# Kernel tuning notes

Measured on AMD Instinct MI355X. Metric: run time of the kernel, lower is better.

## Reference

```python
import jax, jax.numpy as jnp
import numpy as np


def setup_inputs() -> dict:
    key = jax.random.key(0)
    k1, k2, k3, k4 = jax.random.split(key, 4)
    B, T, E, H = 8, 2048, 1024, 64
    x = jax.random.normal(k1, (B, T, E), dtype=jnp.float32)
    # scale params like typical init to keep logits sane
    Wk = jax.random.normal(k2, (E, H), dtype=jnp.float32) * (E ** -0.5)
    Wq = jax.random.normal(k3, (E, H), dtype=jnp.float32) * (E ** -0.5)
    Wv = jax.random.normal(k4, (E, H), dtype=jnp.float32) * (E ** -0.5)
    return {"x": x, "Wk": Wk, "Wq": Wq, "Wv": Wv}


def reference(x, Wk, Wq, Wv):
    # x: [B, T, E]; Wk/Wq/Wv: [E, H]
    T = x.shape[1]
    H = Wk.shape[1]
    k = jnp.einsum('bte,eh->bth', x, Wk)
    q = jnp.einsum('bte,eh->bth', x, Wq)
    v = jnp.einsum('bte,eh->bth', x, Wv)
    # scaled scores [B, T, T]
    wei = jnp.einsum('bqh,bkh->bqk', q, k) * (H ** -0.5)
    causal = jnp.tril(jnp.ones((T, T), dtype=bool))  # tril buffer
    wei = jnp.where(causal, wei, -jnp.inf)
    wei = jax.nn.softmax(wei, axis=-1)
    # dropout p=0.0 (eval): identity
    return jnp.einsum('bqk,bkh->bqh', wei, v)
```

## Files before the change

kernel.cpp:

```cpp
#include <hip/hip_runtime.h>
#include <math.h>

constexpr int B_ = 8, T_ = 2048, E_ = 1024, H_ = 64;
constexpr long BT = (long)B_ * T_;

typedef __attribute__((ext_vector_type(8))) short bf16x8;
typedef __attribute__((ext_vector_type(4))) float f32x4;

__device__ inline unsigned short bf16_rne(float f) {
    union { float f; unsigned u; } v; v.f = f;
    unsigned u = v.u + (0x7FFFu + ((v.u >> 16) & 1u));
    return (unsigned short)(u >> 16);
}
__device__ inline unsigned pack_bf16x2(float lo, float hi) {
    return (unsigned)bf16_rne(lo) | ((unsigned)bf16_rne(hi) << 16);
}

constexpr float QS = 0.18033688011112042f;

__global__ __launch_bounds__(256) void wt_build_k(
    const float* __restrict__ Wk, const float* __restrict__ Wq,
    const float* __restrict__ Wv, unsigned short* __restrict__ Wt)
{
    const int d    = blockIdx.x * 256 + threadIdx.x;
    const int tile = d >> 6;
    const int lq   = d & 63;
    const int quad = lq >> 4;
    const int l16  = lq & 15;
    const int kc   = tile / 12;
    const int nt   = tile - kc * 12;
    const int n    = nt * 16 + l16;

    const float* src; int col; float s = 1.0f;
    if (n < 64)       { src = Wk; col = n; }
    else if (n < 128) { src = Wq; col = n - 64; s = QS; }
    else              { src = Wv; col = n - 128; }

    const int kk0 = kc * 32 + quad * 8;
    const float* sp = src + (size_t)kk0 * H_ + col;
    unsigned p[4];
    #pragma unroll
    for (int jj = 0; jj < 4; jj++)
        p[jj] = pack_bf16x2(sp[(2 * jj) * H_] * s, sp[(2 * jj + 1) * H_] * s);
    *(uint4*)(Wt + (size_t)d * 8) = make_uint4(p[0], p[1], p[2], p[3]);
}

__global__ __launch_bounds__(512, 4) void qkv_mfma_k(
    const float* __restrict__ x, const unsigned short* __restrict__ Wt,
    unsigned short* __restrict__ kO, unsigned short* __restrict__ qO,
    unsigned short* __restrict__ vfO)
{
    __shared__ unsigned short VL[32][66];

    const int t    = threadIdx.x;
    const int w    = t >> 6;
    const int l    = t & 63;
    const int l16  = l & 15;
    const int quad = l >> 4;
    const int rg   = w >> 2;
    const int nq   = w & 3;
    const int row0 = blockIdx.x * 32 + rg * 16;

    const float* xp = x + (size_t)(row0 + l16) * E_ + quad * 8;
    const unsigned short* wp = Wt + (size_t)(nq * 3) * 512 + (size_t)l * 8;

    f32x4 acc[3];
    #pragma unroll
    for (int n = 0; n < 3; n++) acc[n] = (f32x4){0.f, 0.f, 0.f, 0.f};

    float4 a0 = *(const float4*)(xp);
    float4 a1 = *(const float4*)(xp + 4);
    bf16x8 bf[3];
    #pragma unroll
    for (int n = 0; n < 3; n++) bf[n] = *(const bf16x8*)(wp + (size_t)n * 512);

    for (int kc = 0; kc < 32; ++kc) {
        const int kn = (kc + 1) & 31;
        float4 na0 = *(const float4*)(xp + kn * 32);
        float4 na1 = *(const float4*)(xp + kn * 32 + 4);
        bf16x8 nb[3];
        #pragma unroll
        for (int n = 0; n < 3; n++)
            nb[n] = *(const bf16x8*)(wp + (size_t)(kn * 12 + n) * 512);

        union { bf16x8 v; unsigned u[4]; } av;
        av.u[0] = pack_bf16x2(a0.x, a0.y);
        av.u[1] = pack_bf16x2(a0.z, a0.w);
        av.u[2] = pack_bf16x2(a1.x, a1.y);
        av.u[3] = pack_bf16x2(a1.z, a1.w);

        #pragma unroll
        for (int n = 0; n < 3; n++)
            acc[n] = __builtin_amdgcn_mfma_f32_16x16x32_bf16(av.v, bf[n], acc[n], 0, 0, 0);

        a0 = na0; a1 = na1;
        #pragma unroll
        for (int n = 0; n < 3; n++) bf[n] = nb[n];
    }

    #pragma unroll
    for (int n = 0; n < 3; n++) {
        const int gn = nq * 3 + n;
        const int hb = gn * 16 + l16;
        if (gn < 4) {
            #pragma unroll
            for (int r = 0; r < 4; r++) {
                const int row = row0 + quad * 4 + r;
                kO[(size_t)row * H_ + hb] = bf16_rne(acc[n][r]);
            }
        } else if (gn < 8) {
            #pragma unroll
            for (int r = 0; r < 4; r++) {
                const int row = row0 + quad * 4 + r;
                qO[(size_t)row * H_ + (hb - 64)] = bf16_rne(acc[n][r]);
            }
        } else {
            #pragma unroll
            for (int r = 0; r < 4; r++)
                VL[rg * 16 + quad * 4 + r][(gn - 8) * 16 + l16] = bf16_rne(acc[n][r]);
        }
    }
    __syncthreads();

    if (t < 256) {
        const int g  = t >> 6;
        const int lf = t & 15;
        const int qf = (t >> 4) & 3;
        unsigned pk[4];
        #pragma unroll
        for (int jj = 0; jj < 4; jj++) {
            const int p0 = qf * 8 + 2 * jj;
            const int i0 = (p0 >> 1) | ((p0 & 1) << 4);
            const int p1 = p0 + 1;
            const int i1 = (p1 >> 1) | ((p1 & 1) << 4);
            pk[jj] = (unsigned)VL[i0][g * 16 + lf]
                   | ((unsigned)VL[i1][g * 16 + lf] << 16);
        }
        const int tile = blockIdx.x;
        *(uint4*)(vfO + ((size_t)tile * 4 + g) * 512 + (size_t)(t & 63) * 8) =
            make_uint4(pk[0], pk[1], pk[2], pk[3]);
    }
}

__global__ __launch_bounds__(256, 4) void attn_mfma(
    const unsigned short* __restrict__ q,
    const unsigned short* __restrict__ k,
    const unsigned short* __restrict__ vf,
    float* __restrict__ out)
{
    __shared__ unsigned short Pl[4][16 * 40];
    __shared__ float Ot[4][16][68];
    __shared__ float lsW[4][16];

    const int t    = threadIdx.x;
    const int w    = t >> 6;
    const int l    = t & 63;
    const int l16  = l & 15;
    const int quad = l >> 4;

    const int b    = blockIdx.x & 7;
    const int qidx = blockIdx.x >> 3;
    const int qt   = (qidx & 1) ? (127 - (qidx >> 1)) : (qidx >> 1);
    const int t0   = qt * 16;
    const int nk   = t0 / 32 + 1;

    const size_t qoff = ((size_t)b * T_ + t0 + l16) * H_ + quad * 8;
    bf16x8 aq0 = *(const bf16x8*)(q + qoff);
    bf16x8 aq1 = *(const bf16x8*)(q + qoff + 32);

    f32x4 o[4];
    #pragma unroll
    for (int g = 0; g < 4; g++) o[g] = (f32x4){0.f, 0.f, 0.f, 0.f};
    float ls[4] = {0.f, 0.f, 0.f, 0.f};

    const unsigned short* kbp = k + (size_t)b * T_ * H_;
    const unsigned short* vbp = vf + (size_t)b * 64 * 2048 + (size_t)l * 8;
    unsigned short* Pw = &Pl[w][0];

    bf16x8 bk00, bk01, bk10, bk11, bv0, bv1, bv2, bv3;
    if (w < nk) {
        const int kbase = w * 32;
        const unsigned short* kp = kbp + (size_t)(kbase + l16) * H_ + quad * 8;
        bk00 = *(const bf16x8*)(kp);
        bk01 = *(const bf16x8*)(kp + 32);
        bk10 = *(const bf16x8*)(kp + 16 * H_);
        bk11 = *(const bf16x8*)(kp + 16 * H_ + 32);
        const unsigned short* vp = vbp + (size_t)w * 2048;
        bv0 = *(const bf16x8*)(vp);
        bv1 = *(const bf16x8*)(vp + 512);
        bv2 = *(const bf16x8*)(vp + 1024);
        bv3 = *(const bf16x8*)(vp + 1536);
    }

    for (int kt = w; kt < nk; kt += 4) {
        const int ktn    = (kt + 4 < nk) ? kt + 4 : kt;
        const int kbasen = ktn * 32;
        const unsigned short* kpn = kbp + (size_t)(kbasen + l16) * H_ + quad * 8;
        bf16x8 nk00 = *(const bf16x8*)(kpn);
        bf16x8 nk01 = *(const bf16x8*)(kpn + 32);
        bf16x8 nk10 = *(const bf16x8*)(kpn + 16 * H_);
        bf16x8 nk11 = *(const bf16x8*)(kpn + 16 * H_ + 32);
        const unsigned short* vpn = vbp + (size_t)ktn * 2048;
        bf16x8 nv0 = *(const bf16x8*)(vpn);
        bf16x8 nv1 = *(const bf16x8*)(vpn + 512);
        bf16x8 nv2 = *(const bf16x8*)(vpn + 1024);
        bf16x8 nv3 = *(const bf16x8*)(vpn + 1536);

        const int kbase = kt * 32;
        f32x4 s0 = (f32x4){0.f, 0.f, 0.f, 0.f};
        f32x4 s1 = (f32x4){0.f, 0.f, 0.f, 0.f};
        s0 = __builtin_amdgcn_mfma_f32_16x16x32_bf16(aq0, bk00, s0, 0, 0, 0);
        s0 = __builtin_amdgcn_mfma_f32_16x16x32_bf16(aq1, bk01, s0, 0, 0, 0);
        s1 = __builtin_amdgcn_mfma_f32_16x16x32_bf16(aq0, bk10, s1, 0, 0, 0);
        s1 = __builtin_amdgcn_mfma_f32_16x16x32_bf16(aq1, bk11, s1, 0, 0, 0);

        if (kbase + 31 > t0) {
            const int rowb = t0 + quad * 4;
            #pragma unroll
            for (int r = 0; r < 4; r++) {
                if (kbase + l16 > rowb + r)      s0[r] = -3.0e38f;
                if (kbase + 16 + l16 > rowb + r) s1[r] = -3.0e38f;
            }
        }

        #pragma unroll
        for (int r = 0; r < 4; r++) {
            float p0 = exp2f(s0[r]);
            float p1 = exp2f(s1[r]);
            ls[r] += p0 + p1;
            *(unsigned*)(Pw + (quad * 4 + r) * 40 + 2 * l16) = pack_bf16x2(p0, p1);
        }
        asm volatile("s_waitcnt lgkmcnt(0)" ::: "memory");
        bf16x8 ap = *(const bf16x8*)(Pw + l16 * 40 + quad * 8);

        o[0] = __builtin_amdgcn_mfma_f32_16x16x32_bf16(ap, bv0, o[0], 0, 0, 0);
        o[1] = __builtin_amdgcn_mfma_f32_16x16x32_bf16(ap, bv1, o[1], 0, 0, 0);
        o[2] = __builtin_amdgcn_mfma_f32_16x16x32_bf16(ap, bv2, o[2], 0, 0, 0);
        o[3] = __builtin_amdgcn_mfma_f32_16x16x32_bf16(ap, bv3, o[3], 0, 0, 0);

        bk00 = nk00; bk01 = nk01; bk10 = nk10; bk11 = nk11;
        bv0 = nv0; bv1 = nv1; bv2 = nv2; bv3 = nv3;
    }

    #pragma unroll
    for (int r = 0; r < 4; r++) {
        float s = ls[r];
        s += __shfl_xor(s, 1);
        s += __shfl_xor(s, 2);
        s += __shfl_xor(s, 4);
        s += __shfl_xor(s, 8);
        ls[r] = s;
    }
    if (l16 == 0) {
        #pragma unroll
        for (int r = 0; r < 4; r++) lsW[w][quad * 4 + r] = ls[r];
    }
    #pragma unroll
    for (int g = 0; g < 4; g++)
        #pragma unroll
        for (int r = 0; r < 4; r++)
            Ot[w][quad * 4 + r][g * 16 + l16] = o[g][r];
    __syncthreads();

    {
        const int col = w * 16 + l16;
        #pragma unroll
        for (int r = 0; r < 4; r++) {
            const int row = quad * 4 + r;
            float L  = lsW[0][row] + lsW[1][row] + lsW[2][row] + lsW[3][row];
            float sv = Ot[0][row][col] + Ot[1][row][col]
                     + Ot[2][row][col] + Ot[3][row][col];
            out[((size_t)b * T_ + t0 + row) * H_ + col] = sv / L;
        }
    }
}

extern "C" void kernel_launch(void* const* d_in, const int* in_sizes, int n_in,
                              void* d_out, int out_size, void* d_ws, size_t ws_size,
                              hipStream_t stream)
{
    const float* x  = (const float*)d_in[0];
    const float* Wk = (const float*)d_in[1];
    const float* Wq = (const float*)d_in[2];
    const float* Wv = (const float*)d_in[3];

    unsigned short* wt    = (unsigned short*)d_ws;
    unsigned short* kbuf  = wt + 24576 * 8;
    unsigned short* qbuf  = kbuf + BT * H_;
    unsigned short* vfbuf = qbuf + BT * H_;
    float* outp = (float*)d_out;

    wt_build_k<<<96, 256, 0, stream>>>(Wk, Wq, Wv, wt);
    qkv_mfma_k<<<(B_ * T_) / 32, 512, 0, stream>>>(x, wt, kbuf, qbuf, vfbuf);
    attn_mfma<<<B_ * 128, 256, 0, stream>>>(qbuf, kbuf, vfbuf, outp);
}
```

Before: 168.7 us.

## Stage x tiles in LDS via async global_load_lds with double buffering

The QKV projection kernel now copies each 32x64 fp32 tile of x into shared memory with global_load_lds, using a double buffer and an XOR swizzle, instead of having each wave load its own x fragments from global memory straight into registers. Previously the four waves covering different output column groups each fetched the same x rows; sharing one LDS copy removes those duplicate global loads. The cost is a __syncthreads per 64-column step and more LDS use, which can lower occupancy. Weight prefetching into registers is dropped in favour of loads issued inside the loop.

```diff
diff --git a/kernel.cpp b/kernel.cpp
--- a/kernel.cpp
+++ b/kernel.cpp
@@ -14,6 +14,13 @@
 }
 __device__ inline unsigned pack_bf16x2(float lo, float hi) {
     return (unsigned)bf16_rne(lo) | ((unsigned)bf16_rne(hi) << 16);
+}
+
+__device__ inline void load_lds16(const void* g, void* l) {
+    __builtin_amdgcn_global_load_lds(
+        (const __attribute__((address_space(1))) void*)(uintptr_t)g,
+        (__attribute__((address_space(3))) void*)(unsigned)(uintptr_t)l,
+        16, 0, 0);
 }
 
 constexpr float QS = 0.18033688011112042f;
@@ -50,6 +57,7 @@
     unsigned short* __restrict__ kO, unsigned short* __restrict__ qO,
     unsigned short* __restrict__ vfO)
 {
+    __shared__ float4 xs[2][32][16];
     __shared__ unsigned short VL[32][66];
 
     const int t    = threadIdx.x;
@@ -60,42 +68,50 @@
     const int rg   = w >> 2;
     const int nq   = w & 3;
     const int row0 = blockIdx.x * 32 + rg * 16;
-
-    const float* xp = x + (size_t)(row0 + l16) * E_ + quad * 8;
-    const unsigned short* wp = Wt + (size_t)(nq * 3) * 512 + (size_t)l * 8;
+    const int row0b = blockIdx.x * 32;
+
+    const int rr = w * 4 + (l >> 4);
+    const int cc = l & 15;
+    const int gg = cc ^ (rr & 7);
+    const float* gsrc = x + (size_t)(row0b + rr) * E_ + gg * 4;
+
+    const int r  = rg * 16 + l16;
+    const int rx = r & 7;
 
     f32x4 acc[3];
     #pragma unroll
     for (int n = 0; n < 3; n++) acc[n] = (f32x4){0.f, 0.f, 0.f, 0.f};
 
-    float4 a0 = *(const float4*)(xp);
-    float4 a1 = *(const float4*)(xp + 4);
-    bf16x8 bf[3];
-    #pragma unroll
-    for (int n = 0; n < 3; n++) bf[n] = *(const bf16x8*)(wp + (size_t)n * 512);
-
-    for (int kc = 0; kc < 32; ++kc) {
-        const int kn = (kc + 1) & 31;
-        float4 na0 = *(const float4*)(xp + kn * 32);
-        float4 na1 = *(const float4*)(xp + kn * 32 + 4);
-        bf16x8 nb[3];
-        #pragma unroll
-        for (int n = 0; n < 3; n++)
-            nb[n] = *(const bf16x8*)(wp + (size_t)(kn * 12 + n) * 512);
-
-        union { bf16x8 v; unsigned u[4]; } av;
-        av.u[0] = pack_bf16x2(a0.x, a0.y);
-        av.u[1] = pack_bf16x2(a0.z, a0.w);
-        av.u[2] = pack_bf16x2(a1.x, a1.y);
-        av.u[3] = pack_bf16x2(a1.z, a1.w);
-
-        #pragma unroll
-        for (int n = 0; n < 3; n++)
-            acc[n] = __builtin_amdgcn_mfma_f32_16x16x32_bf16(av.v, bf[n], acc[n], 0, 0, 0);
-
-        a0 = na0; a1 = na1;
-        #pragma unroll
-        for (int n = 0; n < 3; n++) bf[n] = nb[n];
+    load_lds16(gsrc, &xs[0][rr][cc]);
+
+    for (int it = 0; it < 16; ++it) {
+        const int buf = it & 1;
+        __syncthreads();
+        if (it + 1 < 16)
+            load_lds16(gsrc + (it + 1) * 64, &xs[buf ^ 1][rr][cc]);
+
+        #pragma unroll
+        for (int kk = 0; kk < 2; ++kk) {
+            const int G0 = kk * 8 + quad * 2;
+            float4 fa = xs[buf][r][G0 ^ rx];
+            float4 fb = xs[buf][r][(G0 + 1) ^ rx];
+
+            const int kc = it * 2 + kk;
+            const unsigned short* wpp = Wt + (size_t)(kc * 12 + nq * 3) * 512 + (size_t)l * 8;
+            bf16x8 b0 = *(const bf16x8*)(wpp);
+            bf16x8 b1 = *(const bf16x8*)(wpp + 512);
+            bf16x8 b2 = *(const bf16x8*)(wpp + 1024);
+
+            union { bf16x8 v; unsigned u[4]; } av;
+            av.u[0] = pack_bf16x2(fa.x, fa.y);
+            av.u[1] = pack_bf16x2(fa.z, fa.w);
+            av.u[2] = pack_bf16x2(fb.x, fb.y);
+            av.u[3] = pack_bf16x2(fb.z, fb.w);
+
+            acc[0] = __builtin_amdgcn_mfma_f32_16x16x32_bf16(av.v, b0, acc[0], 0, 0, 0);
+            acc[1] = __builtin_amdgcn_mfma_f32_16x16x32_bf16(av.v, b1, acc[1], 0, 0, 0);
+            acc[2] = __builtin_amdgcn_mfma_f32_16x16x32_bf16(av.v, b2, acc[2], 0, 0, 0);
+        }
     }
 
     #pragma unroll
@@ -104,20 +120,20 @@
         const int hb = gn * 16 + l16;
         if (gn < 4) {
             #pragma unroll
-            for (int r = 0; r < 4; r++) {
-                const int row = row0 + quad * 4 + r;
-                kO[(size_t)row * H_ + hb] = bf16_rne(acc[n][r]);
+            for (int rr2 = 0; rr2 < 4; rr2++) {
+                const int row = row0 + quad * 4 + rr2;
+                kO[(size_t)row * H_ + hb] = bf16_rne(acc[n][rr2]);
             }
         } else if (gn < 8) {
             #pragma unroll
-            for (int r = 0; r < 4; r++) {
-                const int row = row0 + quad * 4 + r;
-                qO[(size_t)row * H_ + (hb - 64)] = bf16_rne(acc[n][r]);
+            for (int rr2 = 0; rr2 < 4; rr2++) {
+                const int row = row0 + quad * 4 + rr2;
+                qO[(size_t)row * H_ + (hb - 64)] = bf16_rne(acc[n][rr2]);
             }
         } else {
             #pragma unroll
-            for (int r = 0; r < 4; r++)
-                VL[rg * 16 + quad * 4 + r][(gn - 8) * 16 + l16] = bf16_rne(acc[n][r]);
+            for (int rr2 = 0; rr2 < 4; rr2++)
+                VL[rg * 16 + quad * 4 + rr2][(gn - 8) * 16 + l16] = bf16_rne(acc[n][rr2]);
         }
     }
     __syncthreads();
```

Result: faster. 150.0 us (-11.1%).
